# Kernel tuning notes

Measured on AMD Instinct MI355X. Metric: run time of the kernel, lower is better.

Reference implementation:

```python
import jax, jax.numpy as jnp
import numpy as np

B, S, D, KC = 32, 4096, 64, 256  # batch*heads, seq_len, head_dim, compressed dim


def setup_inputs() -> dict:
    key = jax.random.key(0)
    ks = jax.random.split(key, 7)
    return {
        "Q": jax.random.normal(ks[0], (B, S, D), dtype=jnp.float32),
        "K": jax.random.normal(ks[1], (B, S, D), dtype=jnp.float32),
        "V": jax.random.normal(ks[2], (B, S, D), dtype=jnp.float32),
        "E_w": jax.random.normal(ks[3], (KC, S), dtype=jnp.float32) * (1.0 / np.sqrt(S)),
        "E_b": jax.random.normal(ks[4], (KC,), dtype=jnp.float32) * 0.01,
        "F_w": jax.random.normal(ks[5], (KC, S), dtype=jnp.float32) * (1.0 / np.sqrt(S)),
        "F_b": jax.random.normal(ks[6], (KC,), dtype=jnp.float32) * 0.01,
    }


def reference(Q, K, V, E_w, E_b, F_w, F_b):
    # K: [B,S,D] -> transpose -> [B,D,S]; E proj over seq axis -> [B,D,KC]
    Ke = jnp.einsum("bsd,ks->bdk", K, E_w) + E_b  # [B, D, KC]
    # scores: Q @ E(K) -> [B, S, KC], scaled by sqrt(head_dim)
    scale = jnp.sqrt(jnp.asarray(D, dtype=Q.dtype))
    P = jnp.einsum("bsd,bdk->bsk", Q, Ke) / scale
    # causal mask: torch.triu(ones(S, KC)) keeps (i, j) where j >= i
    i = jnp.arange(S)[:, None]
    j = jnp.arange(KC)[None, :]
    keep = j >= i  # [S, KC]
    P = jnp.where(keep[None, :, :], P, jnp.asarray(-1e10, dtype=P.dtype))
    P = jax.nn.softmax(P, axis=-1)  # dropout p=0.0 -> identity
    # V: [B,S,D] -> [B,D,S]; F proj -> [B,D,KC]; transpose -> [B,KC,D]
    Vf = jnp.einsum("bsd,ks->bkd", V, F_w) + F_b[None, :, None]  # [B, KC, D]
    out = jnp.einsum("bsk,bkd->bsd", P, Vf)  # [B, S, D]
    return out
```

## Files before the change

### kernel.cpp

```cpp
#include <hip/hip_runtime.h>
#include <hip/hip_bf16.h>
#include <math.h>

#define NB  32
#define NS  4096
#define ND  64
#define NKC 256
#define ASTR 72
#define PBSTR 264
#define VSTR  264

typedef __attribute__((ext_vector_type(8))) short short8;
typedef __attribute__((ext_vector_type(4))) float f32x4;

__device__ __forceinline__ short f2bf(float f) {
    union { float f; unsigned u; } v; v.f = f;
    return (short)((v.u + 0x7FFFu + ((v.u >> 16) & 1u)) >> 16);
}

__global__ __launch_bounds__(256) void prep(
    const float* __restrict__ Ew, const float* __restrict__ Fw,
    float4* __restrict__ zws, short* __restrict__ EwB, short* __restrict__ FwB)
{
    const int gid = blockIdx.x * 256 + threadIdx.x;
    zws[gid] = (float4){0.f, 0.f, 0.f, 0.f};

    const int half = (NKC * NS) / 8;
    const float* src = (gid < half) ? Ew : Fw;
    short* dst       = (gid < half) ? EwB : FwB;
    const int i8 = (gid < half) ? gid : gid - half;
    float4 a = *(const float4*)&src[(size_t)i8 * 8];
    float4 c = *(const float4*)&src[(size_t)i8 * 8 + 4];
    short8 w;
    w[0] = f2bf(a.x); w[1] = f2bf(a.y); w[2] = f2bf(a.z); w[3] = f2bf(a.w);
    w[4] = f2bf(c.x); w[5] = f2bf(c.y); w[6] = f2bf(c.z); w[7] = f2bf(c.w);
    *(short8*)&dst[(size_t)i8 * 8] = w;
}

template <typename AT>
__global__ __launch_bounds__(256) void proj_gemm(
    const AT* __restrict__ EwX, const AT* __restrict__ FwX,
    const float* __restrict__ K, const float* __restrict__ V,
    float* __restrict__ KeT, float* __restrict__ Vf)
{
    const int x = blockIdx.x, b = blockIdx.y;
    const int chunk = x >> 1, mm = x & 1;
    const AT* __restrict__ Ab    = mm ? FwX : EwX;
    const float* __restrict__ Bg = mm ? V   : K;
    float* __restrict__ Cout     = mm ? Vf  : KeT;

    const int t = threadIdx.x, wave = t >> 6, lane = t & 63;
    const int lm = lane & 15, g = lane >> 4;
    __shared__ short As[256 * ASTR];
    __shared__ short Bs[64 * ASTR];
    const size_t bBase = (size_t)b * NS * ND;
    const int rA = t >> 3, jA = t & 7;
    const int dB = t & 31, sB = t >> 5;

    f32x4 acc[4][4];
#pragma unroll
    for (int mt = 0; mt < 4; ++mt)
#pragma unroll
        for (int nt = 0; nt < 4; ++nt) acc[mt][nt] = (f32x4){0.f, 0.f, 0.f, 0.f};

    const int sBeg = chunk * 512, sEnd = sBeg + 512;
    short8 pa[8];
    float4 paf[16];
    float2 pb[8];
#pragma unroll
    for (int i = 0; i < 8; ++i) {
        if constexpr (sizeof(AT) == 2) {
            pa[i] = *(const short8*)&Ab[(size_t)(i * 32 + rA) * NS + sBeg + jA * 8];
        } else {
            paf[2 * i]     = *(const float4*)&Ab[(size_t)(i * 32 + rA) * NS + sBeg + jA * 8];
            paf[2 * i + 1] = *(const float4*)&Ab[(size_t)(i * 32 + rA) * NS + sBeg + jA * 8 + 4];
        }
    }
#pragma unroll
    for (int i = 0; i < 8; ++i)
        pb[i] = *(const float2*)&Bg[bBase + (size_t)(sBeg + sB * 8 + i) * ND + dB * 2];

    for (int s0 = sBeg; s0 < sEnd; s0 += 64) {
#pragma unroll
        for (int i = 0; i < 8; ++i) {
            if constexpr (sizeof(AT) == 2) {
                *(short8*)&As[(i * 32 + rA) * ASTR + jA * 8] = pa[i];
            } else {
                short8 w;
                w[0] = f2bf(paf[2 * i].x);     w[1] = f2bf(paf[2 * i].y);
                w[2] = f2bf(paf[2 * i].z);     w[3] = f2bf(paf[2 * i].w);
                w[4] = f2bf(paf[2 * i + 1].x); w[5] = f2bf(paf[2 * i + 1].y);
                w[6] = f2bf(paf[2 * i + 1].z); w[7] = f2bf(paf[2 * i + 1].w);
                *(short8*)&As[(i * 32 + rA) * ASTR + jA * 8] = w;
            }
        }
        {
            short8 w0, w1;
#pragma unroll
            for (int i = 0; i < 8; ++i) { w0[i] = f2bf(pb[i].x); w1[i] = f2bf(pb[i].y); }
            *(short8*)&Bs[(dB * 2 + 0) * ASTR + sB * 8] = w0;
            *(short8*)&Bs[(dB * 2 + 1) * ASTR + sB * 8] = w1;
        }
        __syncthreads();
        if (s0 + 64 < sEnd) {
#pragma unroll
            for (int i = 0; i < 8; ++i) {
                if constexpr (sizeof(AT) == 2) {
                    pa[i] = *(const short8*)&Ab[(size_t)(i * 32 + rA) * NS + s0 + 64 + jA * 8];
                } else {
                    paf[2 * i]     = *(const float4*)&Ab[(size_t)(i * 32 + rA) * NS + s0 + 64 + jA * 8];
                    paf[2 * i + 1] = *(const float4*)&Ab[(size_t)(i * 32 + rA) * NS + s0 + 64 + jA * 8 + 4];
                }
            }
#pragma unroll
            for (int i = 0; i < 8; ++i)
                pb[i] = *(const float2*)&Bg[bBase + (size_t)(s0 + 64 + sB * 8 + i) * ND + dB * 2];
        }
#pragma unroll
        for (int ks = 0; ks < 64; ks += 32) {
            short8 aF[4];
#pragma unroll
            for (int mt = 0; mt < 4; ++mt)
                aF[mt] = *(const short8*)&As[(mt * 64 + wave * 16 + lm) * ASTR + ks + g * 8];
#pragma unroll
            for (int nt = 0; nt < 4; ++nt) {
                short8 bF = *(const short8*)&Bs[(nt * 16 + lm) * ASTR + ks + g * 8];
#pragma unroll
                for (int mt = 0; mt < 4; ++mt)
                    acc[mt][nt] = __builtin_amdgcn_mfma_f32_16x16x32_bf16(aF[mt], bF, acc[mt][nt], 0, 0, 0);
            }
        }
        __syncthreads();
    }
#pragma unroll
    for (int mt = 0; mt < 4; ++mt)
#pragma unroll
        for (int r = 0; r < 4; ++r) {
            int kc = mt * 64 + wave * 16 + g * 4 + r;
#pragma unroll
            for (int nt = 0; nt < 4; ++nt)
                atomicAdd(&Cout[((size_t)b * NKC + kc) * ND + nt * 16 + lm], acc[mt][nt][r]);
        }
}

__global__ __launch_bounds__(256) void attn_fused(
    const float* __restrict__ Q,  const float* __restrict__ KeT,
    const float* __restrict__ Vf, const float* __restrict__ Eb,
    const float* __restrict__ Fb, float* __restrict__ out)
{
    const int x = blockIdx.x, b = blockIdx.y, t = threadIdx.x;

    if (x >= 8) {
        __shared__ float pq[16][64];
        __shared__ float mv[64];
        const int kg = t >> 4, dq = t & 15;
        float4 s4 = (float4){0.f, 0.f, 0.f, 0.f};
        for (int p = 0; p < 16; ++p) {
            int k = p * 16 + kg;
            float4 v = *(const float4*)&Vf[((size_t)b * NKC + k) * ND + dq * 4];
            float fb = Fb[k];
            s4.x += v.x + fb; s4.y += v.y + fb; s4.z += v.z + fb; s4.w += v.w + fb;
        }
        *(float4*)&pq[kg][dq * 4] = s4;
        __syncthreads();
        if (t < 64) {
            float m = 0.f;
#pragma unroll
            for (int i = 0; i < 16; ++i) m += pq[i][t];
            mv[t] = m * (1.f / 256.f);
        }
        __syncthreads();
        const int r0 = 256 + (x - 8) * 64;
#pragma unroll
        for (int i = 0; i < 4; ++i) {
            int idx = i * 256 + t, row = idx >> 4, q = idx & 15;
            *(float4*)&out[((size_t)b * NS + r0 + row) * ND + q * 4] =
                *(const float4*)&mv[q * 4];
        }
        return;
    }

    const int s0 = x * 32;
    const int wave = t >> 6, lane = t & 63, lm = lane & 15, g = lane >> 4;
    __shared__ short Qs[32 * ASTR];
    __shared__ short PsB[32 * PBSTR];
    __shared__ short VfT[64 * VSTR];
    __shared__ float rsums[32][4];

    {
        int row = t >> 3, dq = t & 7;
        size_t off = ((size_t)b * NS + s0 + row) * ND + dq * 8;
        float4 q0 = *(const float4*)&Q[off], q1 = *(const float4*)&Q[off + 4];
        short8 w;
        w[0] = f2bf(q0.x); w[1] = f2bf(q0.y); w[2] = f2bf(q0.z); w[3] = f2bf(q0.w);
        w[4] = f2bf(q1.x); w[5] = f2bf(q1.y); w[6] = f2bf(q1.z); w[7] = f2bf(q1.w);
        *(short8*)&Qs[row * ASTR + dq * 8] = w;
    }
    {
        const int dB = t & 31, sB = t >> 5;
#pragma unroll
        for (int pass = 0; pass < 4; ++pass) {
            int kb = pass * 64 + sB * 8;
            float2 v[8]; float fb[8];
#pragma unroll
            for (int i = 0; i < 8; ++i) {
                v[i]  = *(const float2*)&Vf[((size_t)b * NKC + kb + i) * ND + dB * 2];
                fb[i] = Fb[kb + i];
            }
            short8 w0, w1;
#pragma unroll
            for (int i = 0; i < 8; ++i) {
                w0[i] = f2bf(v[i].x + fb[i]);
                w1[i] = f2bf(v[i].y + fb[i]);
            }
            *(short8*)&VfT[(dB * 2 + 0) * VSTR + kb] = w0;
            *(short8*)&VfT[(dB * 2 + 1) * VSTR + kb] = w1;
        }
    }
    __syncthreads();

    f32x4 accP[2][4];
#pragma unroll
    for (int rt = 0; rt < 2; ++rt)
#pragma unroll
        for (int kk = 0; kk < 4; ++kk) accP[rt][kk] = (f32x4){0.f, 0.f, 0.f, 0.f};
#pragma unroll
    for (int kk = 0; kk < 4; ++kk) {
        int kt = wave * 4 + kk;
        float ebv = Eb[kt * 16 + lm];
#pragma unroll
        for (int ks2 = 0; ks2 < 2; ++ks2) {
            const float* kp = &KeT[((size_t)b * NKC + kt * 16 + lm) * ND + ks2 * 32 + g * 8];
            float4 c0 = *(const float4*)kp, c1 = *(const float4*)(kp + 4);
            short8 bf;
            bf[0] = f2bf(c0.x + ebv); bf[1] = f2bf(c0.y + ebv);
            bf[2] = f2bf(c0.z + ebv); bf[3] = f2bf(c0.w + ebv);
            bf[4] = f2bf(c1.x + ebv); bf[5] = f2bf(c1.y + ebv);
            bf[6] = f2bf(c1.z + ebv); bf[7] = f2bf(c1.w + ebv);
#pragma unroll
            for (int rt = 0; rt < 2; ++rt) {
                short8 aq = *(const short8*)&Qs[(rt * 16 + lm) * ASTR + ks2 * 32 + g * 8];
                accP[rt][kk] = __builtin_amdgcn_mfma_f32_16x16x32_bf16(aq, bf, accP[rt][kk], 0, 0, 0);
            }
        }
    }
#pragma unroll
    for (int rt = 0; rt < 2; ++rt)
#pragma unroll
        for (int r = 0; r < 4; ++r) {
            float s = 0.f;
            int rowg = s0 + rt * 16 + g * 4 + r;
#pragma unroll
            for (int kk = 0; kk < 4; ++kk) {
                int col = wave * 64 + kk * 16 + lm;
                float e = (col >= rowg) ? __expf(accP[rt][kk][r] * 0.125f) : 0.f;
                accP[rt][kk][r] = e;
                s += e;
            }
#pragma unroll
            for (int off = 1; off <= 8; off <<= 1) s += __shfl_xor(s, off, 64);
            if (lm == 0) rsums[rt * 16 + g * 4 + r][wave] = s;
        }
    __syncthreads();
#pragma unroll
    for (int rt = 0; rt < 2; ++rt)
#pragma unroll
        for (int r = 0; r < 4; ++r) {
            float4 rs = *(const float4*)&rsums[rt * 16 + g * 4 + r][0];
            float inv = 1.f / (rs.x + rs.y + rs.z + rs.w);
#pragma unroll
            for (int kk = 0; kk < 4; ++kk)
                PsB[(rt * 16 + g * 4 + r) * PBSTR + wave * 64 + kk * 16 + lm] =
                    f2bf(accP[rt][kk][r] * inv);
        }
    __syncthreads();

    f32x4 oa[2];
    oa[0] = (f32x4){0.f, 0.f, 0.f, 0.f};
    oa[1] = (f32x4){0.f, 0.f, 0.f, 0.f};
    for (int ks = x; ks < 8; ++ks) {
        short8 bv = *(const short8*)&VfT[(wave * 16 + lm) * VSTR + ks * 32 + g * 8];
#pragma unroll
        for (int rt = 0; rt < 2; ++rt) {
            short8 av = *(const short8*)&PsB[(rt * 16 + lm) * PBSTR + ks * 32 + g * 8];
            oa[rt] = __builtin_amdgcn_mfma_f32_16x16x32_bf16(av, bv, oa[rt], 0, 0, 0);
        }
    }
#pragma unroll
    for (int rt = 0; rt < 2; ++rt)
#pragma unroll
        for (int r = 0; r < 4; ++r)
            out[((size_t)b * NS + s0 + rt * 16 + g * 4 + r) * ND + wave * 16 + lm] = oa[rt][r];
}

extern "C" void kernel_launch(void* const* d_in, const int* in_sizes, int n_in,
                              void* d_out, int out_size, void* d_ws, size_t ws_size,
                              hipStream_t stream) {
    (void)in_sizes; (void)n_in; (void)out_size;
    const float* Q  = (const float*)d_in[0];
    const float* K  = (const float*)d_in[1];
    const float* V  = (const float*)d_in[2];
    const float* Ew = (const float*)d_in[3];
    const float* Eb = (const float*)d_in[4];
    const float* Fw = (const float*)d_in[5];
    const float* Fb = (const float*)d_in[6];
    float* out = (float*)d_out;

    const size_t nKe = (size_t)NB * NKC * ND;
    float* KeT = (float*)d_ws;
    float* Vf  = KeT + nKe;

    if (ws_size >= 8u * 1024 * 1024) {
        short* EwB = (short*)(Vf + nKe);
        short* FwB = EwB + (size_t)NKC * NS;
        prep<<<dim3(1024), 256, 0, stream>>>(Ew, Fw, (float4*)d_ws, EwB, FwB);
        proj_gemm<short><<<dim3(16, NB), 256, 0, stream>>>(EwB, FwB, K, V, KeT, Vf);
    } else {
        hipMemsetAsync(d_ws, 0, 2 * nKe * sizeof(float), stream);
        proj_gemm<float><<<dim3(16, NB), 256, 0, stream>>>(Ew, Fw, K, V, KeT, Vf);
    }
    attn_fused<<<dim3(68, NB), 256, 0, stream>>>(Q, KeT, Vf, Eb, Fb, out);
}
```

Before: 177.7 us.

## Replace split-K projection GEMM with full-K output tiles, dropping atomics and zeroing

The projection GEMM no longer splits the sequence reduction across blocks. Each of 256 blocks now owns one (batch, matrix, 64-row KC tile) and loops over the full sequence with a 128-wide K step, writing results directly with plain stores. This removes the float atomicAdds, the workspace zeroing in prep, and the memset on the fallback path. In exchange, each K/V slice is loaded and converted to bf16 four times (once per KC tile), and each block runs a long serial loop with fewer MFMAs per iteration and low occupancy.

```diff
diff --git a/kernel.cpp b/kernel.cpp
--- a/kernel.cpp
+++ b/kernel.cpp
@@ -6,7 +6,12 @@
 #define NS  4096
 #define ND  64
 #define NKC 256
-#define ASTR 72
+
+#define BK   128
+#define ASA  132
+#define ASB  132
+
+#define QSTR  72
 #define PBSTR 264
 #define VSTR  264
 
@@ -20,11 +25,9 @@
 
 __global__ __launch_bounds__(256) void prep(
     const float* __restrict__ Ew, const float* __restrict__ Fw,
-    float4* __restrict__ zws, short* __restrict__ EwB, short* __restrict__ FwB)
+    short* __restrict__ EwB, short* __restrict__ FwB)
 {
     const int gid = blockIdx.x * 256 + threadIdx.x;
-    zws[gid] = (float4){0.f, 0.f, 0.f, 0.f};
-
     const int half = (NKC * NS) / 8;
     const float* src = (gid < half) ? Ew : Fw;
     short* dst       = (gid < half) ? EwB : FwB;
@@ -43,103 +46,109 @@
     const float* __restrict__ K, const float* __restrict__ V,
     float* __restrict__ KeT, float* __restrict__ Vf)
 {
-    const int x = blockIdx.x, b = blockIdx.y;
-    const int chunk = x >> 1, mm = x & 1;
+    const int bid = blockIdx.x;
+    const int r8 = bid & 7, mt = (bid >> 3) & 3, G = bid >> 5;
+    const int g  = G * 8 + r8, b = g >> 1, mm = g & 1;
+
     const AT* __restrict__ Ab    = mm ? FwX : EwX;
     const float* __restrict__ Bg = mm ? V   : K;
     float* __restrict__ Cout     = mm ? Vf  : KeT;
 
     const int t = threadIdx.x, wave = t >> 6, lane = t & 63;
-    const int lm = lane & 15, g = lane >> 4;
-    __shared__ short As[256 * ASTR];
-    __shared__ short Bs[64 * ASTR];
+    const int lm = lane & 15, g4 = lane >> 4;
+    __shared__ short As[64 * ASA];
+    __shared__ short Bs[64 * ASB];
     const size_t bBase = (size_t)b * NS * ND;
-    const int rA = t >> 3, jA = t & 7;
+    const size_t aBase = (size_t)mt * 64 * NS;
+    const int rA = t >> 4, jA = t & 15;
     const int dB = t & 31, sB = t >> 5;
 
-    f32x4 acc[4][4];
-#pragma unroll
-    for (int mt = 0; mt < 4; ++mt)
-#pragma unroll
-        for (int nt = 0; nt < 4; ++nt) acc[mt][nt] = (f32x4){0.f, 0.f, 0.f, 0.f};
-
-    const int sBeg = chunk * 512, sEnd = sBeg + 512;
-    short8 pa[8];
-    float4 paf[16];
-    float2 pb[8];
-#pragma unroll
-    for (int i = 0; i < 8; ++i) {
+    f32x4 acc[4];
+#pragma unroll
+    for (int nt = 0; nt < 4; ++nt) acc[nt] = (f32x4){0.f, 0.f, 0.f, 0.f};
+
+    short8 pa[4];
+    float4 paf[8];
+    float2 pb[16];
+
+#pragma unroll
+    for (int i = 0; i < 4; ++i) {
         if constexpr (sizeof(AT) == 2) {
-            pa[i] = *(const short8*)&Ab[(size_t)(i * 32 + rA) * NS + sBeg + jA * 8];
+            pa[i] = *(const short8*)&Ab[aBase + (size_t)(i * 16 + rA) * NS + jA * 8];
         } else {
-            paf[2 * i]     = *(const float4*)&Ab[(size_t)(i * 32 + rA) * NS + sBeg + jA * 8];
-            paf[2 * i + 1] = *(const float4*)&Ab[(size_t)(i * 32 + rA) * NS + sBeg + jA * 8 + 4];
-        }
-    }
-#pragma unroll
-    for (int i = 0; i < 8; ++i)
-        pb[i] = *(const float2*)&Bg[bBase + (size_t)(sBeg + sB * 8 + i) * ND + dB * 2];
-
-    for (int s0 = sBeg; s0 < sEnd; s0 += 64) {
-#pragma unroll
-        for (int i = 0; i < 8; ++i) {
+            paf[2 * i]     = *(const float4*)&Ab[aBase + (size_t)(i * 16 + rA) * NS + jA * 8];
+            paf[2 * i + 1] = *(const float4*)&Ab[aBase + (size_t)(i * 16 + rA) * NS + jA * 8 + 4];
+        }
+    }
+#pragma unroll
+    for (int h = 0; h < 2; ++h)
+#pragma unroll
+        for (int i = 0; i < 8; ++i)
+            pb[h * 8 + i] = *(const float2*)&Bg[bBase + (size_t)(h * 64 + sB * 8 + i) * ND + dB * 2];
+
+    for (int s0 = 0; s0 < NS; s0 += BK) {
+#pragma unroll
+        for (int i = 0; i < 4; ++i) {
             if constexpr (sizeof(AT) == 2) {
-                *(short8*)&As[(i * 32 + rA) * ASTR + jA * 8] = pa[i];
+                *(short8*)&As[(i * 16 + rA) * ASA + jA * 8] = pa[i];
             } else {
                 short8 w;
                 w[0] = f2bf(paf[2 * i].x);     w[1] = f2bf(paf[2 * i].y);
                 w[2] = f2bf(paf[2 * i].z);     w[3] = f2bf(paf[2 * i].w);
                 w[4] = f2bf(paf[2 * i + 1].x); w[5] = f2bf(paf[2 * i + 1].y);
                 w[6] = f2bf(paf[2 * i + 1].z); w[7] = f2bf(paf[2 * i + 1].w);
-                *(short8*)&As[(i * 32 + rA) * ASTR + jA * 8] = w;
-            }
-        }
-        {
+                *(short8*)&As[(i * 16 + rA) * ASA + jA * 8] = w;
+            }
+        }
+#pragma unroll
+        for (int h = 0; h < 2; ++h) {
             short8 w0, w1;
 #pragma unroll
-            for (int i = 0; i < 8; ++i) { w0[i] = f2bf(pb[i].x); w1[i] = f2bf(pb[i].y); }
-            *(short8*)&Bs[(dB * 2 + 0) * ASTR + sB * 8] = w0;
-            *(short8*)&Bs[(dB * 2 + 1) * ASTR + sB * 8] = w1;
+            for (int i = 0; i < 8; ++i) {
+                w0[i] = f2bf(pb[h * 8 + i].x);
+                w1[i] = f2bf(pb[h * 8 + i].y);
+            }
+            *(short8*)&Bs[(dB * 2 + 0) * ASB + h * 64 + sB * 8] = w0;
+            *(short8*)&Bs[(dB * 2 + 1) * ASB + h * 64 + sB * 8] = w1;
         }
         __syncthreads();
-        if (s0 + 64 < sEnd) {
-#pragma unroll
-            for (int i = 0; i < 8; ++i) {
+
+        if (s0 + BK < NS) {
+            const int sn = s0 + BK;
+#pragma unroll
+            for (int i = 0; i < 4; ++i) {
                 if constexpr (sizeof(AT) == 2) {
-                    pa[i] = *(const short8*)&Ab[(size_t)(i * 32 + rA) * NS + s0 + 64 + jA * 8];
+                    pa[i] = *(const short8*)&Ab[aBase + (size_t)(i * 16 + rA) * NS + sn + jA * 8];
                 } else {
-                    paf[2 * i]     = *(const float4*)&Ab[(size_t)(i * 32 + rA) * NS + s0 + 64 + jA * 8];
-                    paf[2 * i + 1] = *(const float4*)&Ab[(size_t)(i * 32 + rA) * NS + s0 + 64 + jA * 8 + 4];
+                    paf[2 * i]     = *(const float4*)&Ab[aBase + (size_t)(i * 16 + rA) * NS + sn + jA * 8];
+                    paf[2 * i + 1] = *(const float4*)&Ab[aBase + (size_t)(i * 16 + rA) * NS + sn + jA * 8 + 4];
                 }
             }
 #pragma unroll
-            for (int i = 0; i < 8; ++i)
-                pb[i] = *(const float2*)&Bg[bBase + (size_t)(s0 + 64 + sB * 8 + i) * ND + dB * 2];
-        }
-#pragma unroll
-        for (int ks = 0; ks < 64; ks += 32) {
-            short8 aF[4];
-#pragma unroll
-            for (int mt = 0; mt < 4; ++mt)
-                aF[mt] = *(const short8*)&As[(mt * 64 + wave * 16 + lm) * ASTR + ks + g * 8];
+            for (int h = 0; h < 2; ++h)
+#pragma unroll
+                for (int i = 0; i < 8; ++i)
+                    pb[h * 8 + i] = *(const float2*)&Bg[bBase + (size_t)(sn + h * 64 + sB * 8 + i) * ND + dB * 2];
+        }
+
+#pragma unroll
+        for (int ks = 0; ks < BK; ks += 32) {
+            short8 aF = *(const short8*)&As[(wave * 16 + lm) * ASA + ks + g4 * 8];
 #pragma unroll
             for (int nt = 0; nt < 4; ++nt) {
-                short8 bF = *(const short8*)&Bs[(nt * 16 + lm) * ASTR + ks + g * 8];
-#pragma unroll
-                for (int mt = 0; mt < 4; ++mt)
-                    acc[mt][nt] = __builtin_amdgcn_mfma_f32_16x16x32_bf16(aF[mt], bF, acc[mt][nt], 0, 0, 0);
+                short8 bF = *(const short8*)&Bs[(nt * 16 + lm) * ASB + ks + g4 * 8];
+                acc[nt] = __builtin_amdgcn_mfma_f32_16x16x32_bf16(aF, bF, acc[nt], 0, 0, 0);
             }
         }
         __syncthreads();
     }
-#pragma unroll
-    for (int mt = 0; mt < 4; ++mt)
-#pragma unroll
-        for (int r = 0; r < 4; ++r) {
-            int kc = mt * 64 + wave * 16 + g * 4 + r;
-#pragma unroll
-            for (int nt = 0; nt < 4; ++nt)
-                atomicAdd(&Cout[((size_t)b * NKC + kc) * ND + nt * 16 + lm], acc[mt][nt][r]);
+
+#pragma unroll
+    for (int nt = 0; nt < 4; ++nt)
+#pragma unroll
+        for (int rr = 0; rr < 4; ++rr) {
+            int kc = mt * 64 + wave * 16 + g4 * 4 + rr;
+            Cout[((size_t)b * NKC + kc) * ND + nt * 16 + lm] = acc[nt][rr];
         }
 }
 
@@ -182,7 +191,7 @@
 
     const int s0 = x * 32;
     const int wave = t >> 6, lane = t & 63, lm = lane & 15, g = lane >> 4;
-    __shared__ short Qs[32 * ASTR];
+    __shared__ short Qs[32 * QSTR];
     __shared__ short PsB[32 * PBSTR];
     __shared__ short VfT[64 * VSTR];
     __shared__ float rsums[32][4];
@@ -194,7 +203,7 @@
         short8 w;
         w[0] = f2bf(q0.x); w[1] = f2bf(q0.y); w[2] = f2bf(q0.z); w[3] = f2bf(q0.w);
         w[4] = f2bf(q1.x); w[5] = f2bf(q1.y); w[6] = f2bf(q1.z); w[7] = f2bf(q1.w);
-        *(short8*)&Qs[row * ASTR + dq * 8] = w;
+        *(short8*)&Qs[row * QSTR + dq * 8] = w;
     }
     {
         const int dB = t & 31, sB = t >> 5;
@@ -239,7 +248,7 @@
             bf[6] = f2bf(c1.z + ebv); bf[7] = f2bf(c1.w + ebv);
 #pragma unroll
             for (int rt = 0; rt < 2; ++rt) {
-                short8 aq = *(const short8*)&Qs[(rt * 16 + lm) * ASTR + ks2 * 32 + g * 8];
+                short8 aq = *(const short8*)&Qs[(rt * 16 + lm) * QSTR + ks2 * 32 + g * 8];
                 accP[rt][kk] = __builtin_amdgcn_mfma_f32_16x16x32_bf16(aq, bf, accP[rt][kk], 0, 0, 0);
             }
         }
@@ -313,11 +322,10 @@
     if (ws_size >= 8u * 1024 * 1024) {
         short* EwB = (short*)(Vf + nKe);
         short* FwB = EwB + (size_t)NKC * NS;
-        prep<<<dim3(1024), 256, 0, stream>>>(Ew, Fw, (float4*)d_ws, EwB, FwB);
-        proj_gemm<short><<<dim3(16, NB), 256, 0, stream>>>(EwB, FwB, K, V, KeT, Vf);
+        prep<<<dim3(1024), 256, 0, stream>>>(Ew, Fw, EwB, FwB);
+        proj_gemm<short><<<dim3(256), 256, 0, stream>>>(EwB, FwB, K, V, KeT, Vf);
     } else {
-        hipMemsetAsync(d_ws, 0, 2 * nKe * sizeof(float), stream);
-        proj_gemm<float><<<dim3(16, NB), 256, 0, stream>>>(Ew, Fw, K, V, KeT, Vf);
+        proj_gemm<float><<<dim3(256), 256, 0, stream>>>(Ew, Fw, K, V, KeT, Vf);
     }
     attn_fused<<<dim3(68, NB), 256, 0, stream>>>(Q, KeT, Vf, Eb, Fb, out);
 }
```

Result: slower. 195.3 us (+9.9%).
